# Kernel tuning notes

Measured on AMD Instinct MI355X. Metric: run time of the kernel, lower is better.

## Reference

```python
import jax, jax.numpy as jnp
from jax import lax
import numpy as np

B, Q, C = 128, 200, 92  # batch, num_queries, num_classes (0 = no-object)


def hungarian(cost):
    """Exact Hungarian assignment (augmenting-path / JV potentials, e-maxx form).
    cost: [n, n]. Returns col_of_row: [n] int32, the column matched to each row.
    Uses 1-based columns/rows internally; index 0 is the sentinel."""
    n = cost.shape[0]
    INF = jnp.asarray(1e9, cost.dtype)

    def solve_row(i, carry):
        u, v, p = carry
        p = p.at[0].set(jnp.int32(i))
        minv = jnp.full(n + 1, INF, cost.dtype)
        way = jnp.zeros(n + 1, jnp.int32)
        used = jnp.zeros(n + 1, bool)
        state = (u, v, p, minv, way, used, jnp.int32(0))

        def cond(s):
            _u, _v, _p, _minv, _way, _used, j0 = s
            return _p[j0] != 0

        def body(s):
            u, v, p, minv, way, used, j0 = s
            used = used.at[j0].set(True)
            i0 = p[j0]
            cur = cost[i0 - 1, :] - u[i0] - v[1:]          # reduced costs of row i0
            cur = jnp.where(used[1:], INF, cur)
            upd = cur < minv[1:]
            minv = minv.at[1:].set(jnp.where(upd, cur, minv[1:]))
            way = way.at[1:].set(jnp.where(upd, j0, way[1:]))
            masked = jnp.where(used[1:], INF, minv[1:])
            j1 = jnp.argmin(masked).astype(jnp.int32) + 1
            delta = masked[j1 - 1]
            zero = jnp.asarray(0, cost.dtype)
            u = u.at[p].add(jnp.where(used, delta, zero))  # u[p[j]] += delta for used j (rows distinct)
            v = jnp.where(used, v - delta, v)
            minv = jnp.where(used, minv, minv - delta)
            return (u, v, p, minv, way, used, j1)

        u, v, p, minv, way, used, j0 = lax.while_loop(cond, body, state)

        def aug_body(s):  # flip matching along the alternating path
            p, j0 = s
            j1 = way[j0]
            return p.at[j0].set(p[j1]), j1

        p, _ = lax.while_loop(lambda s: s[1] != 0, aug_body, (p, j0))
        return (u, v, p)

    u0 = jnp.zeros(n + 1, cost.dtype)
    v0 = jnp.zeros(n + 1, cost.dtype)
    p0 = jnp.zeros(n + 1, jnp.int32)
    _, _, p = lax.fori_loop(1, n + 1, solve_row, (u0, v0, p0))
    # p[j] = row matched to column j (1-based); invert to col per row (0-based)
    col_of_row = jnp.zeros(n, jnp.int32).at[p[1:] - 1].set(jnp.arange(n, dtype=jnp.int32))
    return col_of_row


def cost_matrix(pred_cat, pred_bbox, tar_cat, tar_bbox):
    b, q, c = pred_cat.shape
    log_probs = jax.nn.log_softmax(pred_cat, axis=-1)                  # [B,Qp,C]
    idx = jnp.broadcast_to(tar_cat[:, None, :], (b, q, q))             # [B,Qp,Qt]
    ce = -jnp.take_along_axis(log_probs, idx, axis=2)                  # CE(pred_i, tgt_j)
    d = pred_bbox[:, :, None, :] - tar_bbox[:, None, :, :]             # [B,Qp,Qt,4]
    ad = jnp.abs(d)
    sl1 = jnp.where(ad < 1.0, 0.5 * d * d, ad - 0.5).sum(-1)           # SmoothL1 (beta=1)
    mask = (tar_cat != 0).astype(sl1.dtype)[:, None, :]                # bbox loss only for real objects
    return ce + sl1 * mask                                             # [B,Qp,Qt]


def setup_inputs() -> dict:
    key = jax.random.key(0)
    k1, k2, k3, k4 = jax.random.split(key, 4)
    pred_cat = jax.random.normal(k1, (B, Q, C), dtype=jnp.float32)
    pred_bbox = jax.random.uniform(k2, (B, Q, 4), dtype=jnp.float32)
    tar_cat = jax.random.randint(k3, (B, Q), 0, C, dtype=jnp.int32)
    tar_bbox = jax.random.uniform(k4, (B, Q, 4), dtype=jnp.float32)
    return {"pred_cat": pred_cat, "pred_bbox": pred_bbox, "tar_cat": tar_cat, "tar_bbox": tar_bbox}


def reference(pred_cat, pred_bbox, tar_cat, tar_bbox):
    cost = cost_matrix(pred_cat, pred_bbox, tar_cat, tar_bbox)         # [B,Q,Q]
    col = jax.vmap(hungarian)(lax.stop_gradient(cost))                 # assignment on detached cost
    out = jnp.take_along_axis(cost, col[:, :, None], axis=2)[..., 0]   # [B,Q] per-query matched loss
    return out
```

## Files before the change

### kernel.cpp

```cpp
#include <hip/hip_runtime.h>
#include <math.h>

#define BB 128
#define QQ 200
#define CC 92
#define CMPAD (QQ * QQ + 64)

__global__ void lse_kernel(const float* __restrict__ pc, float* __restrict__ lse) {
    int idx = blockIdx.x * blockDim.x + threadIdx.x;
    if (idx >= BB * QQ) return;
    const float* row = pc + (size_t)idx * CC;
    float m = -INFINITY;
    for (int c = 0; c < CC; ++c) m = fmaxf(m, row[c]);
    float s = 0.f;
    for (int c = 0; c < CC; ++c) s += expf(row[c] - m);
    lse[idx] = m + logf(s);
}

__global__ void cost_kernel(const float* __restrict__ pc,
                            const float* __restrict__ pb,
                            const int*   __restrict__ tc,
                            const float* __restrict__ tb,
                            const float* __restrict__ lse,
                            float* __restrict__ cost) {
    long idx = blockIdx.x * (long)blockDim.x + threadIdx.x;
    if (idx >= (long)BB * QQ * QQ) return;
    int j = (int)(idx % QQ);
    int i = (int)((idx / QQ) % QQ);
    int b = (int)(idx / ((long)QQ * QQ));
    int cls = tc[b * QQ + j];
    float ce = lse[b * QQ + i] - pc[((size_t)(b * QQ + i)) * CC + cls];
    const float* pbb = pb + ((size_t)(b * QQ + i)) * 4;
    const float* tbb = tb + ((size_t)(b * QQ + j)) * 4;
    float sl1 = 0.f;
#pragma unroll
    for (int k = 0; k < 4; ++k) {
        float d = pbb[k] - tbb[k];
        float ad = fabsf(d);
        sl1 += (ad < 1.f) ? 0.5f * d * d : (ad - 0.5f);
    }
    float mask = (cls != 0) ? 1.f : 0.f;
    cost[idx] = ce + sl1 * mask;
}

__device__ __forceinline__ int rdlane_i(int x, int l) { return __builtin_amdgcn_readlane(x, l); }
__device__ __forceinline__ float rdlane_f(float x, int l) {
    return __uint_as_float((unsigned)__builtin_amdgcn_readlane((int)__float_as_uint(x), l));
}

__device__ __forceinline__ float wave_fmin_bcast(float x) {
    float y;
#define DPPSTEP(ctrl) \
    y = __uint_as_float((unsigned)__builtin_amdgcn_update_dpp( \
            (int)__float_as_uint(x), (int)__float_as_uint(x), ctrl, 0xf, 0xf, false)); \
    x = fminf(x, y);
    DPPSTEP(0x111) DPPSTEP(0x112) DPPSTEP(0x114) DPPSTEP(0x118)
    DPPSTEP(0x142) DPPSTEP(0x143)
#undef DPPSTEP
    return rdlane_f(x, 63);
}

__global__ __launch_bounds__(64) void hungarian_kernel(const float* __restrict__ cost,
                                                       float* __restrict__ out) {
    const int b = blockIdx.x;
    const int t = threadIdx.x;
    const float* cb = cost + (size_t)b * QQ * QQ;

    __shared__ __align__(16) float cm[CMPAD];

    {
        const float4* src = (const float4*)cb;
        float4* dst = (float4*)cm;
        for (int idx = t; idx < QQ * QQ / 4; idx += 64) dst[idx] = src[idx];
    }

    const float INF = 1e9f;
    const int nval = (t < 8) ? 4 : 3;

    float v[4]     = {0.f, 0.f, 0.f, 0.f};
    int   pslot[4] = {0, 0, 0, 0};
    float uslot[4] = {0.f, 0.f, 0.f, 0.f};
    float minv[4];
    int   waysl[4];
    int   usedm;
    float usent;

    for (int i = 1; i <= QQ; ++i) {
        minv[0] = minv[1] = minv[2] = minv[3] = INF;
        waysl[0] = waysl[1] = waysl[2] = waysl[3] = 0;
        usedm = 0;
        usent = 0.f;
        int j0 = 0;
        float u0 = 0.f;
        const float* crow = cm + (i - 1) * QQ;
        float c0 = crow[t];
        float c1 = crow[64 + t];
        float c2 = crow[128 + t];
        float c3 = crow[192 + t];

        for (;;) {
            if (j0 > 0) {
                int s = (j0 - 1) >> 6;
                if (((j0 - 1) & 63) == t) usedm |= 1 << s;
            }

            float kv0, kv1, kv2, kv3;
            {
                float cur;
                cur = c0 - u0 - v[0];
                if (!(usedm & 1) && cur < minv[0]) { minv[0] = cur; waysl[0] = j0; }
                kv0 = (usedm & 1) ? INF : minv[0];
                cur = c1 - u0 - v[1];
                if (!(usedm & 2) && cur < minv[1]) { minv[1] = cur; waysl[1] = j0; }
                kv1 = (usedm & 2) ? INF : minv[1];
                cur = c2 - u0 - v[2];
                if (!(usedm & 4) && cur < minv[2]) { minv[2] = cur; waysl[2] = j0; }
                kv2 = (usedm & 4) ? INF : minv[2];
                cur = c3 - u0 - v[3];
                if (!(usedm & 8) && t < 8 && cur < minv[3]) { minv[3] = cur; waysl[3] = j0; }
                kv3 = ((usedm & 8) || t >= 8) ? INF : minv[3];
            }

            float gmin = wave_fmin_bcast(fminf(fminf(kv0, kv1), fminf(kv2, kv3)));
            float delta = gmin;

            unsigned long long m0 = __ballot(kv0 == gmin);
            unsigned long long m1 = __ballot(kv1 == gmin);
            unsigned long long m2 = __ballot(kv2 == gmin);
            unsigned long long m3 = __ballot(kv3 == gmin);
            int j1;
            if (m0)      j1 = 1   + (int)__builtin_ctzll(m0);
            else if (m1) j1 = 65  + (int)__builtin_ctzll(m1);
            else if (m2) j1 = 129 + (int)__builtin_ctzll(m2);
            else         j1 = 193 + (int)__builtin_ctzll(m3);

            int kk = (j1 - 1) >> 6, ln = (j1 - 1) & 63;
            int   ps = (kk == 0) ? pslot[0] : (kk == 1) ? pslot[1]
                      : (kk == 2) ? pslot[2] : pslot[3];
            float us = (kk == 0) ? uslot[0] : (kk == 1) ? uslot[1]
                      : (kk == 2) ? uslot[2] : uslot[3];
            int pi = rdlane_i(ps, ln);

            int nr = (pi > 0 ? pi : 1) - 1;
            const float* nrow = cm + nr * QQ;
            float n0 = nrow[t];
            float n1 = nrow[64 + t];
            float n2 = nrow[128 + t];
            float n3 = nrow[192 + t];

            float u0n = rdlane_f(us, ln);

#pragma unroll
            for (int k = 0; k < 4; ++k) {
                if (usedm & (1 << k)) {
                    v[k] -= delta;
                    uslot[k] += delta;
                } else if (k < nval) {
                    minv[k] -= delta;
                }
            }
            usent += delta;

            if (pi == 0) { j0 = j1; break; }
            j0 = j1; u0 = u0n;
            c0 = n0; c1 = n1; c2 = n2; c3 = n3;
        }

        {
            int jj = j0;
            while (jj != 0) {
                int jm = jj - 1, km = jm >> 6, lm = jm & 63;
                int ws = (km == 0) ? waysl[0] : (km == 1) ? waysl[1]
                        : (km == 2) ? waysl[2] : waysl[3];
                int jn = rdlane_i(ws, lm);
                int pnew; float unew;
                if (jn == 0) {
                    pnew = i;
                    unew = usent;
                } else {
                    int jm2 = jn - 1, kn = jm2 >> 6, ln2 = jm2 & 63;
                    int   ps2 = (kn == 0) ? pslot[0] : (kn == 1) ? pslot[1]
                               : (kn == 2) ? pslot[2] : pslot[3];
                    float us2 = (kn == 0) ? uslot[0] : (kn == 1) ? uslot[1]
                               : (kn == 2) ? uslot[2] : uslot[3];
                    pnew = rdlane_i(ps2, ln2);
                    unew = rdlane_f(us2, ln2);
                }
                if (lm == t) { pslot[km] = pnew; uslot[km] = unew; }
                jj = jn;
            }
        }
    }

#pragma unroll
    for (int k = 0; k < 4; ++k) {
        if (k < nval) {
            int jc = 1 + t + 64 * k;
            int row = pslot[k] - 1;
            out[b * QQ + row] = cm[row * QQ + (jc - 1)];
        }
    }
}

extern "C" void kernel_launch(void* const* d_in, const int* in_sizes, int n_in,
                              void* d_out, int out_size, void* d_ws, size_t ws_size,
                              hipStream_t stream) {
    const float* pred_cat  = (const float*)d_in[0];
    const float* pred_bbox = (const float*)d_in[1];
    const int*   tar_cat   = (const int*)d_in[2];
    const float* tar_bbox  = (const float*)d_in[3];
    float* out = (float*)d_out;

    float* cost = (float*)d_ws;
    float* lse  = cost + (size_t)BB * QQ * QQ;

    lse_kernel<<<(BB * QQ + 255) / 256, 256, 0, stream>>>(pred_cat, lse);
    cost_kernel<<<((long)BB * QQ * QQ + 255) / 256, 256, 0, stream>>>(
        pred_cat, pred_bbox, tar_cat, tar_bbox, lse, cost);
    hungarian_kernel<<<BB, 64, 0, stream>>>(cost, out);
}
```

Before: 1.463 ms.

## Fuse log-sum-exp and cost-matrix construction into the Hungarian kernel via LDS

Removes the separate log-sum-exp and cost-matrix kernels and builds each batch's cost matrix directly in shared memory inside the Hungarian kernel. This removes two kernel launches and the write and read-back of the full cost tensor through global memory. In exchange, the per-row log-sum-exp and cost fill now run inside a single 64-thread wave per batch with only 128 blocks, so that part has far less parallelism than before.

```diff
diff --git a/kernel.cpp b/kernel.cpp
--- a/kernel.cpp
+++ b/kernel.cpp
@@ -5,43 +5,6 @@
 #define QQ 200
 #define CC 92
 #define CMPAD (QQ * QQ + 64)
-
-__global__ void lse_kernel(const float* __restrict__ pc, float* __restrict__ lse) {
-    int idx = blockIdx.x * blockDim.x + threadIdx.x;
-    if (idx >= BB * QQ) return;
-    const float* row = pc + (size_t)idx * CC;
-    float m = -INFINITY;
-    for (int c = 0; c < CC; ++c) m = fmaxf(m, row[c]);
-    float s = 0.f;
-    for (int c = 0; c < CC; ++c) s += expf(row[c] - m);
-    lse[idx] = m + logf(s);
-}
-
-__global__ void cost_kernel(const float* __restrict__ pc,
-                            const float* __restrict__ pb,
-                            const int*   __restrict__ tc,
-                            const float* __restrict__ tb,
-                            const float* __restrict__ lse,
-                            float* __restrict__ cost) {
-    long idx = blockIdx.x * (long)blockDim.x + threadIdx.x;
-    if (idx >= (long)BB * QQ * QQ) return;
-    int j = (int)(idx % QQ);
-    int i = (int)((idx / QQ) % QQ);
-    int b = (int)(idx / ((long)QQ * QQ));
-    int cls = tc[b * QQ + j];
-    float ce = lse[b * QQ + i] - pc[((size_t)(b * QQ + i)) * CC + cls];
-    const float* pbb = pb + ((size_t)(b * QQ + i)) * 4;
-    const float* tbb = tb + ((size_t)(b * QQ + j)) * 4;
-    float sl1 = 0.f;
-#pragma unroll
-    for (int k = 0; k < 4; ++k) {
-        float d = pbb[k] - tbb[k];
-        float ad = fabsf(d);
-        sl1 += (ad < 1.f) ? 0.5f * d * d : (ad - 0.5f);
-    }
-    float mask = (cls != 0) ? 1.f : 0.f;
-    cost[idx] = ce + sl1 * mask;
-}
 
 __device__ __forceinline__ int rdlane_i(int x, int l) { return __builtin_amdgcn_readlane(x, l); }
 __device__ __forceinline__ float rdlane_f(float x, int l) {
@@ -60,18 +23,64 @@
     return rdlane_f(x, 63);
 }
 
-__global__ __launch_bounds__(64) void hungarian_kernel(const float* __restrict__ cost,
+__global__ __launch_bounds__(64) void hungarian_kernel(const float* __restrict__ pc,
+                                                       const float* __restrict__ pb,
+                                                       const int*   __restrict__ tc,
+                                                       const float* __restrict__ tb,
                                                        float* __restrict__ out) {
     const int b = blockIdx.x;
     const int t = threadIdx.x;
-    const float* cb = cost + (size_t)b * QQ * QQ;
+    const int base = b * QQ;
 
     __shared__ __align__(16) float cm[CMPAD];
-
-    {
-        const float4* src = (const float4*)cb;
-        float4* dst = (float4*)cm;
-        for (int idx = t; idx < QQ * QQ / 4; idx += 64) dst[idx] = src[idx];
+    __shared__ float lse_s[QQ];
+
+    int    clsk[4];
+    float4 tbbk[4];
+    float  maskk[4];
+#pragma unroll
+    for (int k = 0; k < 4; ++k) {
+        int j = t + 64 * k;
+        if (j < QQ) {
+            clsk[k]  = tc[base + j];
+            tbbk[k]  = *(const float4*)(tb + (size_t)(base + j) * 4);
+            maskk[k] = (clsk[k] != 0) ? 1.f : 0.f;
+        } else {
+            clsk[k] = 0; tbbk[k] = make_float4(0.f, 0.f, 0.f, 0.f); maskk[k] = 0.f;
+        }
+    }
+
+#pragma unroll
+    for (int k = 0; k < 4; ++k) {
+        int r = t + 64 * k;
+        if (r < QQ) {
+            const float* row = pc + (size_t)(base + r) * CC;
+            float m = -INFINITY;
+            for (int c = 0; c < CC; ++c) m = fmaxf(m, row[c]);
+            float s = 0.f;
+            for (int c = 0; c < CC; ++c) s += expf(row[c] - m);
+            lse_s[r] = m + logf(s);
+        }
+    }
+
+    for (int i = 0; i < QQ; ++i) {
+        const float  lsei  = lse_s[i];
+        const float* pcrow = pc + (size_t)(base + i) * CC;
+        const float4 pbb   = *(const float4*)(pb + (size_t)(base + i) * 4);
+        float* cmrow = cm + i * QQ;
+#pragma unroll
+        for (int k = 0; k < 4; ++k) {
+            if (k < 3 || t < 8) {
+                float ce = lsei - pcrow[clsk[k]];
+                float sl1 = 0.f;
+                float d, ad;
+                d = pbb.x - tbbk[k].x; ad = fabsf(d); sl1 += (ad < 1.f) ? 0.5f * d * d : (ad - 0.5f);
+                d = pbb.y - tbbk[k].y; ad = fabsf(d); sl1 += (ad < 1.f) ? 0.5f * d * d : (ad - 0.5f);
+                d = pbb.z - tbbk[k].z; ad = fabsf(d); sl1 += (ad < 1.f) ? 0.5f * d * d : (ad - 0.5f);
+                d = pbb.w - tbbk[k].w; ad = fabsf(d); sl1 += (ad < 1.f) ? 0.5f * d * d : (ad - 0.5f);
+                cmrow[t + 64 * k] = ce + sl1 * maskk[k];
+            }
+        }
     }
 
     const float INF = 1e9f;
@@ -210,12 +219,8 @@
     const int*   tar_cat   = (const int*)d_in[2];
     const float* tar_bbox  = (const float*)d_in[3];
     float* out = (float*)d_out;
-
-    float* cost = (float*)d_ws;
-    float* lse  = cost + (size_t)BB * QQ * QQ;
-
-    lse_kernel<<<(BB * QQ + 255) / 256, 256, 0, stream>>>(pred_cat, lse);
-    cost_kernel<<<((long)BB * QQ * QQ + 255) / 256, 256, 0, stream>>>(
-        pred_cat, pred_bbox, tar_cat, tar_bbox, lse, cost);
-    hungarian_kernel<<<BB, 64, 0, stream>>>(cost, out);
-}
+    (void)d_ws; (void)ws_size;
+
+    hungarian_kernel<<<BB, 64, 0, stream>>>(pred_cat, pred_bbox, tar_cat,
+                                            tar_bbox, out);
+}
```

New measurement: 1.502 ms. +2.7%, slower.
